# Performance work log

Measured on AMD Instinct MI355X. Metric: run time of the kernel, lower is better.

The kernel has to match this reference:

```python
import jax, jax.numpy as jnp
import numpy as np

F32 = jnp.float32

def denorm_px(pts, H, W):
    # kornia denormalize_pixel_coordinates: [-1,1] -> pixel
    x = (pts[..., 0] + 1.0) * (W - 1) * 0.5
    y = (pts[..., 1] + 1.0) * (H - 1) * 0.5
    return jnp.stack([x, y], axis=-1)

def norm_px(pts, H, W):
    x = pts[..., 0] * 2.0 / (W - 1) - 1.0
    y = pts[..., 1] * 2.0 / (H - 1) - 1.0
    return jnp.stack([x, y], axis=-1)

def conv2d_same(x, k, mode):
    # depthwise 2d conv, 'same' output, border via jnp.pad mode
    kh, kw = k.shape
    ph, pw = kh // 2, kw // 2
    xp = jnp.pad(x, ((0, 0), (0, 0), (ph, ph), (pw, pw)), mode=mode)
    C = x.shape[1]
    kern = jnp.broadcast_to(k[None, None], (C, 1, kh, kw)).astype(x.dtype)
    return jax.lax.conv_general_dilated(xp, kern, (1, 1), 'VALID',
        dimension_numbers=('NCHW', 'OIHW', 'NCHW'), feature_group_count=C)

def nms2d(x, k=5):
    p = k // 2
    m = jax.lax.reduce_window(x, -jnp.inf, jax.lax.max, (1, 1, k, k), (1, 1, 1, 1),
                              [(0, 0), (0, 0), (p, p), (p, p)])
    return jnp.where(x == m, x, 0.0)

def gaussian_kernel2d(ksize=7, sigma=1.0):
    ax = jnp.arange(ksize, dtype=F32) - (ksize - 1) / 2.0
    g = jnp.exp(-0.5 * (ax / sigma) ** 2)
    g = g / g.sum()
    return jnp.outer(g, g)

def gftt_response(gray):
    # kornia CornerGFTT: normalized sobel grads, blurred structure tensor, min-eig
    sx = jnp.array([[-1, 0, 1], [-2, 0, 2], [-1, 0, 1]], F32) / 8.0
    gx = conv2d_same(gray, sx, 'edge')
    gy = conv2d_same(gray, sx.T, 'edge')
    g = gaussian_kernel2d(7, 1.0)
    dx2 = conv2d_same(gx * gx, g, 'reflect')
    dy2 = conv2d_same(gy * gy, g, 'reflect')
    dxy = conv2d_same(gx * gy, g, 'reflect')
    tr = dx2 + dy2
    disc = jnp.sqrt(jnp.clip((dx2 - dy2) ** 2 + 4.0 * dxy ** 2, 0.0))
    return 0.5 * (tr - disc)

def laplacian5(x):
    k = jnp.ones((5, 5), F32).at[2, 2].set(1.0 - 25.0)
    k = k / jnp.abs(k).sum()  # kornia normalized laplacian kernel
    return conv2d_same(x, k, 'reflect')

def pairwise_project(pts, depths, poses, K):
    # pts [B,N,2] normalized; poses [B,4,4] cam-to-world
    # returns proj [B(dst),B(src),N,2] normalized + vis [B,B,N]
    B, N, _ = pts.shape
    H, W = depths.shape[-2:]
    px = denorm_px(pts, H, W)
    xi = jnp.clip(jnp.round(px[..., 0]), 0, W - 1).astype(jnp.int32)
    yi = jnp.clip(jnp.round(px[..., 1]), 0, H - 1).astype(jnp.int32)
    d = depths[jnp.arange(B)[:, None], 0, yi, xi]  # [B,N]
    Kinv = jnp.linalg.inv(K)
    hom = jnp.concatenate([px, jnp.ones_like(px[..., :1])], axis=-1)
    cam = (hom @ Kinv.T) * d[..., None]  # [B,N,3]
    R, t = poses[:, :3, :3], poses[:, :3, 3]
    world = jnp.einsum('bij,bnj->bni', R, cam) + t[:, None]
    diff = world[None] - t[:, None, None]  # [i,j,n,3]
    cam2 = jnp.einsum('iab,ijna->ijnb', R, diff)  # R_i^T (world - t_i)
    uvw = cam2 @ K.T
    z = uvw[..., 2]
    zs = jnp.where(jnp.abs(z) > 1e-6, z, 1e-6)
    u, v = uvw[..., 0] / zs, uvw[..., 1] / zs
    vis = (z > 0.1) & (u >= 0) & (u <= W - 1) & (v >= 0) & (v <= H - 1)
    return norm_px(jnp.stack([u, v], -1), H, W), vis

def pairwise_cosine_inter(x, y, eps=1e-8):
    xx = jnp.sum(x * x, -1)
    yy = jnp.sum(y * y, -1)
    xy = jnp.einsum('amd,bnd->abmn', x, y)
    den = jnp.sqrt(jnp.clip(xx[:, None, :, None] * yy[None, :, None, :], eps * eps))
    return xy / den

def pairwise_cosine_intra(x, y, eps=1e-8):
    xx = jnp.sum(x * x, -1)
    yy = jnp.sum(y * y, -1)
    xy = jnp.einsum('bmd,bnd->bmn', x, y)
    den = jnp.sqrt(jnp.clip(xx[..., :, None] * yy[..., None, :], eps * eps))
    return xy / den

def distinction_loss(desc):
    return jnp.maximum(pairwise_cosine_intra(desc, desc), 0.0).mean()

def match_loss(desc, points, proj, vis, H, W, radius=1.0):
    B, N, _ = points.shape
    src = denorm_px(jax.lax.stop_gradient(points), H, W)  # [b,m,2]
    dst = denorm_px(jax.lax.stop_gradient(proj), H, W)  # [a,b,n,2]
    x2 = jnp.sum(src * src, -1)  # [b,m]
    y2 = jnp.sum(dst * dst, -1)  # [a,b,n]
    xy = jnp.einsum('bmd,abnd->abmn', src, dst)
    dist = jnp.sqrt(jnp.clip(x2[None, :, :, None] + y2[:, :, None, :] - 2.0 * xy, 0.0))
    valid = vis[:, :, :, None]  # torch: dist[invis rows] = nan -> excluded from both masks
    tri = jnp.triu(jnp.ones((N, N), bool), 1)
    pcos = pairwise_cosine_inter(desc, desc)
    mpos = (dist <= radius) & tri & valid
    mneg = (dist > radius) & tri & valid
    pos_mean = jnp.sum(jnp.where(mpos, pcos, 0.0)) / jnp.maximum(mpos.sum(), 1)
    neg_mean = jnp.sum(jnp.where(mneg, pcos, 0.0)) / jnp.maximum(mneg.sum(), 1)
    return 1.0 - pos_mean + neg_mean

def get_corner_target(imgs, depths, poses, K, num_corners=500, radius=8):
    B, _, H, W = imgs.shape
    gray = 0.299 * imgs[:, 0:1] + 0.587 * imgs[:, 1:2] + 0.114 * imgs[:, 2:3]
    corners = nms2d(gftt_response(gray), 5)
    # MaxPool(8, return_indices) + MaxUnpool(8): keep only per-8x8-block max
    xr = corners.reshape(B, 1, H // radius, radius, W // radius, radius)
    bm = xr.max(axis=(3, 5), keepdims=True)
    keep = jnp.where(xr == bm, xr, 0.0).reshape(B, 1, H, W)
    values, idx = jax.lax.top_k(keep.reshape(B, -1), num_corners)  # [B,Nc]
    coords = jnp.stack([idx % W, idx // W], axis=2).astype(F32)  # (x,y)
    coords = norm_px(coords, H, W)
    proj, vis = pairwise_project(coords, depths, poses, K)  # [B,B,Nc,2]
    proj = jnp.where(vis[..., None], proj, -2.0)
    comb = jnp.transpose(proj, (1, 0, 2, 3)).reshape(B, B * num_corners, 2)
    px = jnp.round(denorm_px(comb, H, W)).astype(jnp.int32)
    wf = px[..., 0].reshape(-1)
    hf = px[..., 1].reshape(-1)
    bf = jnp.repeat(jnp.arange(B), B * num_corners)
    vals = jnp.tile(values.reshape(-1), B)
    mask = (wf >= 0) & (hf >= 0) & (wf < W) & (hf < H)
    vals = jnp.where(mask, vals, 0.0)
    wf = jnp.clip(wf, 0, W - 1)
    hf = jnp.clip(hf, 0, H - 1)
    target = jnp.zeros_like(corners).at[bf, 0, hf, wf].max(vals)
    target = nms2d(target, 5)
    return jax.lax.stop_gradient((target > 0).astype(F32))

def score_loss(scores, imgs, depths, poses, K):
    target = get_corner_target(imgs, depths, poses, K)
    p = jnp.clip(scores, 1e-12, 1.0 - 1e-12)
    bce = -(target * jnp.log(p) + (1.0 - target) * jnp.log(1.0 - p)).mean()
    lap = laplacian5(scores)
    return bce + (scores * jnp.exp(-lap)).mean() * 10.0

def featurenet_loss(descriptors, points, pointness, depths_dense, poses, K, imgs):
    beta = (1.0, 0.5, 1.0)
    H, W = pointness.shape[2], pointness.shape[3]
    distinction = distinction_loss(descriptors)
    cornerness = score_loss(pointness, imgs, depths_dense, poses, K)
    proj_pts, vis = pairwise_project(points, depths_dense, poses, K)
    match = match_loss(descriptors, points, proj_pts, vis, H, W, radius=1.0)
    return beta[0] * distinction + beta[1] * cornerness + beta[2] * match

def setup_inputs() -> dict:
    key = jax.random.key(0)
    ks = jax.random.split(key, 6)
    B, N, D, H, W = 6, 1024, 128, 320, 320
    descriptors = jax.random.normal(ks[0], (B, N, D), F32)
    points = jax.random.uniform(ks[1], (B, N, 2), F32, -0.9, 0.9)
    pointness = jax.random.uniform(ks[2], (B, 1, H, W), F32, 1e-3, 1.0 - 1e-3)
    depths_dense = jax.random.uniform(ks[3], (B, 1, H, W), F32, 1.0, 6.0)
    t = jax.random.uniform(ks[4], (B, 3), F32, -0.2, 0.2)
    poses = jnp.tile(jnp.eye(4, dtype=F32), (B, 1, 1)).at[:, :3, 3].set(t)
    K = jnp.array([[float(W), 0.0, W / 2.0], [0.0, float(W), H / 2.0], [0.0, 0.0, 1.0]], F32)
    imgs = jax.random.uniform(ks[5], (B, 3, H, W), F32)
    return dict(descriptors=descriptors, points=points, pointness=pointness,
                depths_dense=depths_dense, poses=poses, K=K, imgs=imgs)

def reference(descriptors, points, pointness, depths_dense, poses, K, imgs):
    return featurenet_loss(descriptors, points, pointness, depths_dense, poses, K, imgs)
```

## Files before the change

### kernel.cpp

```cpp
#include <hip/hip_runtime.h>
#include <stdint.h>

#define BB 6
#define NPTS 1024
#define DD 128
#define HH 320
#define WW 320
#define NC 500
#define HWsz (HH*WW)
#define CAP 2048
#define NBLK ((HH/8)*(WW/8))
#define TX 32
#define TY 8
#define NSLOT 64

typedef __attribute__((ext_vector_type(8))) short bf16x8;
typedef __attribute__((ext_vector_type(4))) float f32x4;

__device__ __forceinline__ int clampi(int v, int lo, int hi){ return v<lo?lo:(v>hi?hi:v); }
__device__ __forceinline__ int refl(int p, int L){ if(p<0)p=-p; if(p>=L)p=2*L-2-p; return p; }

__device__ __forceinline__ float wave_sum(float v){
  #pragma unroll
  for (int o = 32; o > 0; o >>= 1) v += __shfl_xor(v, o, 64);
  return v;
}
__device__ __forceinline__ double wave_sumd(double v){
  #pragma unroll
  for (int o = 32; o > 0; o >>= 1) v += __shfl_xor(v, o, 64);
  return v;
}
__device__ __forceinline__ float wave_max(float v){
  #pragma unroll
  for (int o = 32; o > 0; o >>= 1) v = fmaxf(v, __shfl_xor(v, o, 64));
  return v;
}

__device__ __constant__ float GW[7] = {
  0.0044330481f, 0.0540055850f, 0.2420362300f, 0.3990502700f,
  0.2420362300f, 0.0540055850f, 0.0044330481f };

struct Proj { float u, v; int vis; };

__device__ Proj project_point(float ptx, float pty, int jsrc, int itgt,
                              const float* __restrict__ depths,
                              const float* __restrict__ poses,
                              const float* __restrict__ Km)
{
  float pxx = ((ptx + 1.0f)*(float)(WW-1))*0.5f;
  float pxy = ((pty + 1.0f)*(float)(HH-1))*0.5f;
  float rx = rintf(pxx), ry = rintf(pxy);
  rx = fminf(fmaxf(rx, 0.f), (float)(WW-1));
  ry = fminf(fmaxf(ry, 0.f), (float)(HH-1));
  int xi = (int)rx, yi = (int)ry;
  float d = depths[(size_t)jsrc*HWsz + yi*WW + xi];
  float a00=Km[0],a01=Km[1],a02=Km[2],a10=Km[3],a11=Km[4],a12=Km[5],a20=Km[6],a21=Km[7],a22=Km[8];
  float det = a00*(a11*a22 - a12*a21) - a01*(a10*a22 - a12*a20) + a02*(a10*a21 - a11*a20);
  float id_ = 1.0f/det;
  float i00 = (a11*a22 - a12*a21)*id_;
  float i01 = (a02*a21 - a01*a22)*id_;
  float i02 = (a01*a12 - a02*a11)*id_;
  float i10 = (a12*a20 - a10*a22)*id_;
  float i11 = (a00*a22 - a02*a20)*id_;
  float i12 = (a02*a10 - a00*a12)*id_;
  float i20 = (a10*a21 - a11*a20)*id_;
  float i21 = (a01*a20 - a00*a21)*id_;
  float i22 = (a00*a11 - a01*a10)*id_;
  float c0 = (i00*pxx + i01*pxy + i02)*d;
  float c1 = (i10*pxx + i11*pxy + i12)*d;
  float c2 = (i20*pxx + i21*pxy + i22)*d;
  const float* Pj = poses + (size_t)jsrc*16;
  float w0 = Pj[0]*c0 + Pj[1]*c1 + Pj[2]*c2  + Pj[3];
  float w1 = Pj[4]*c0 + Pj[5]*c1 + Pj[6]*c2  + Pj[7];
  float w2 = Pj[8]*c0 + Pj[9]*c1 + Pj[10]*c2 + Pj[11];
  const float* Pi = poses + (size_t)itgt*16;
  float dx = w0 - Pi[3], dy = w1 - Pi[7], dz = w2 - Pi[11];
  float e0 = Pi[0]*dx + Pi[4]*dy + Pi[8]*dz;
  float e1 = Pi[1]*dx + Pi[5]*dy + Pi[9]*dz;
  float e2 = Pi[2]*dx + Pi[6]*dy + Pi[10]*dz;
  float uu = a00*e0 + a01*e1 + a02*e2;
  float vv = a10*e0 + a11*e1 + a12*e2;
  float zz = a20*e0 + a21*e1 + a22*e2;
  float zs = (fabsf(zz) > 1e-6f) ? zz : 1e-6f;
  Proj r;
  r.u = uu/zs; r.v = vv/zs;
  r.vis = (zz > 0.1f) && (r.u >= 0.f) && (r.u <= (float)(WW-1)) && (r.v >= 0.f) && (r.v <= (float)(HH-1));
  return r;
}

__global__ __launch_bounds__(256) void k_graysobel(const float* __restrict__ imgs,
        float* __restrict__ gxx, float* __restrict__ gyy, float* __restrict__ gxy){
  __shared__ float lg[TY+2][TX+2];
  int b = blockIdx.z;
  int x0 = blockIdx.x*TX, y0 = blockIdx.y*TY;
  const float* br = imgs + (size_t)b*3*HWsz;
  const float* bg = br + HWsz;
  const float* bb = bg + HWsz;
  const int W2 = TX+2, H2 = TY+2;
  for (int i = threadIdx.x; i < H2*W2; i += 256){
    int ly = i / W2, lx = i - ly*W2;
    int gy = clampi(y0 - 1 + ly, 0, HH-1), gx = clampi(x0 - 1 + lx, 0, WW-1);
    size_t off = (size_t)gy*WW + gx;
    lg[ly][lx] = 0.299f*br[off] + 0.587f*bg[off] + 0.114f*bb[off];
  }
  __syncthreads();
  int tx = threadIdx.x & (TX-1), ty = threadIdx.x / TX;
  float g00 = lg[ty][tx],   g01 = lg[ty][tx+1],   g02 = lg[ty][tx+2];
  float g10 = lg[ty+1][tx],                        g12 = lg[ty+1][tx+2];
  float g20 = lg[ty+2][tx], g21 = lg[ty+2][tx+1], g22 = lg[ty+2][tx+2];
  float gx = 0.125f*(g02-g00) + 0.25f*(g12-g10) + 0.125f*(g22-g20);
  float gy = 0.125f*(g20-g00) + 0.25f*(g21-g01) + 0.125f*(g22-g02);
  size_t o = (size_t)b*HWsz + (size_t)(y0+ty)*WW + (x0+tx);
  gxx[o] = gx*gx; gyy[o] = gy*gy; gxy[o] = gx*gy;
}

__global__ __launch_bounds__(256) void k_gauss_resp(const float* __restrict__ gxx,
        const float* __restrict__ gyy, const float* __restrict__ gxy, float* __restrict__ resp){
  __shared__ float lxx[TY+6][TX+6], lyy[TY+6][TX+6], lxy[TY+6][TX+6];
  int b = blockIdx.z;
  int x0 = blockIdx.x*TX, y0 = blockIdx.y*TY;
  const float* axx = gxx + (size_t)b*HWsz;
  const float* ayy = gyy + (size_t)b*HWsz;
  const float* axy = gxy + (size_t)b*HWsz;
  const int W2 = TX+6, H2 = TY+6;
  for (int i = threadIdx.x; i < H2*W2; i += 256){
    int ly = i / W2, lx = i - ly*W2;
    int gy = refl(y0 - 3 + ly, HH), gx = refl(x0 - 3 + lx, WW);
    size_t off = (size_t)gy*WW + gx;
    lxx[ly][lx] = axx[off]; lyy[ly][lx] = ayy[off]; lxy[ly][lx] = axy[off];
  }
  __syncthreads();
  int tx = threadIdx.x & (TX-1), ty = threadIdx.x / TX;
  float sxx=0.f, syy=0.f, sxy=0.f;
  #pragma unroll
  for (int i=0;i<7;++i){
    float wr = GW[i];
    #pragma unroll
    for (int j=0;j<7;++j){
      float wc = wr*GW[j];
      sxx += wc*lxx[ty+i][tx+j];
      syy += wc*lyy[ty+i][tx+j];
      sxy += wc*lxy[ty+i][tx+j];
    }
  }
  float tr = sxx+syy, df = sxx-syy;
  float disc = sqrtf(fmaxf(df*df + 4.f*sxy*sxy, 0.f));
  resp[(size_t)b*HWsz + (size_t)(y0+ty)*WW + (x0+tx)] = 0.5f*(tr - disc);
}

__global__ __launch_bounds__(256) void k_nmsblk(const float* __restrict__ resp,
        unsigned long long* __restrict__ ckeys, unsigned int* __restrict__ ccnt){
  __shared__ float lr[TY+4][TX+4];
  __shared__ float lk[TY][TX];
  int b = blockIdx.z;
  int x0 = blockIdx.x*TX, y0 = blockIdx.y*TY;
  const float* rb = resp + (size_t)b*HWsz;
  const int W2 = TX+4, H2 = TY+4;
  for (int i = threadIdx.x; i < H2*W2; i += 256){
    int ly = i / W2, lx = i - ly*W2;
    int gy = y0 - 2 + ly, gx = x0 - 2 + lx;
    lr[ly][lx] = (gy >= 0 && gy < HH && gx >= 0 && gx < WW) ? rb[(size_t)gy*WW + gx] : -1e30f;
  }
  __syncthreads();
  int tx = threadIdx.x & (TX-1), ty = threadIdx.x / TX;
  float m = -1e30f;
  #pragma unroll
  for (int dy=0; dy<5; ++dy)
    #pragma unroll
    for (int dx=0; dx<5; ++dx) m = fmaxf(m, lr[ty+dy][tx+dx]);
  float r = lr[ty+2][tx+2];
  lk[ty][tx] = (r == m) ? r : 0.f;
  __syncthreads();
  int wave = threadIdx.x >> 6, lane = threadIdx.x & 63;
  int ly = lane >> 3, lx = wave*8 + (lane & 7);
  float v = lk[ly][lx];
  float bm = wave_max(v);
  if (!(bm > 0.f)) return;
  unsigned long long mask = __ballot(v == bm);
  if (v == bm){
    int yy = y0 + ly, xx2 = x0 + lx;
    unsigned long long key =
      ((unsigned long long)__float_as_uint(bm) << 32) |
      (unsigned long long)(0xFFFFFFFFu - (unsigned int)(yy*WW + xx2));
    int rank = __popcll(mask & ((1ull << lane) - 1ull));
    int rblk = blockIdx.y*(WW/8) + blockIdx.x*4 + wave;
    if (rank == 0){
      ckeys[(size_t)b*CAP + rblk] = key;
    } else {
      unsigned int slot = NBLK + atomicAdd(&ccnt[b], 1u);
      if (slot < CAP) ckeys[(size_t)b*CAP + slot] = key;
    }
  }
}

__global__ __launch_bounds__(1024) void k_top500(const unsigned long long* __restrict__ ckeys,
        float* __restrict__ cpts, float* __restrict__ cvals){
  __shared__ unsigned long long sk[CAP];
  int b = blockIdx.x;
  int tid = threadIdx.x;
  for (int i = tid; i < CAP; i += 1024)
    sk[i] = ckeys[(size_t)b*CAP + i];
  __syncthreads();
  for (int k = 2; k <= CAP; k <<= 1){
    for (int j = k >> 1; j > 0; j >>= 1){
      for (int i = tid; i < CAP; i += 1024){
        int l = i ^ j;
        if (l > i){
          unsigned long long A = sk[i], Bv = sk[l];
          bool up = ((i & k) == 0);
          if ((A > Bv) == up){ sk[i] = Bv; sk[l] = A; }
        }
      }
      __syncthreads();
    }
  }
  if (tid < NC){
    unsigned long long key = sk[CAP-1-tid];
    float val = __uint_as_float((unsigned int)(key >> 32));
    size_t o = (size_t)b*NC + tid;
    if (val > 0.f){
      unsigned int idx = 0xFFFFFFFFu - (unsigned int)(key & 0xFFFFFFFFull);
      float fx = (float)(idx % WW), fy = (float)(idx / WW);
      cpts[o*2+0] = (fx*2.0f)/(float)(WW-1) - 1.0f;
      cpts[o*2+1] = (fy*2.0f)/(float)(HH-1) - 1.0f;
      cvals[o] = val;
    } else {
      cpts[o*2+0] = __int_as_float(0x7fc00000);
      cpts[o*2+1] = __int_as_float(0x7fc00000);
      cvals[o] = 0.f;
    }
  }
}

__global__ void k_corner_scatter(const float* __restrict__ cpts, const float* __restrict__ cvals,
        const float* __restrict__ depths, const float* __restrict__ poses,
        const float* __restrict__ Km, unsigned int* __restrict__ target){
  int t = blockIdx.x*blockDim.x + threadIdx.x;
  if (t >= BB*BB*NC) return;
  int i = t / (BB*NC); int r = t - i*(BB*NC); int j = r / NC; int n = r - j*NC;
  float val = cvals[(size_t)i*NC + n];
  float ptx = cpts[((size_t)j*NC+n)*2+0];
  float pty = cpts[((size_t)j*NC+n)*2+1];
  if (!(val > 0.f) || ptx != ptx) return;
  Proj pr = project_point(ptx, pty, j, i, depths, poses, Km);
  if (!pr.vis) return;
  float nu = (pr.u*2.0f)/(float)(WW-1) - 1.0f;
  float nv = (pr.v*2.0f)/(float)(HH-1) - 1.0f;
  float px2 = ((nu+1.0f)*(float)(WW-1))*0.5f;
  float py2 = ((nv+1.0f)*(float)(HH-1))*0.5f;
  float rx = rintf(px2), ry = rintf(py2);
  if (!(rx >= 0.f && ry >= 0.f && rx <= (float)(WW-1) && ry <= (float)(HH-1))) return;
  int wf = (int)rx, hf = (int)ry;
  atomicMax(&target[(size_t)j*HWsz + hf*WW + wf], __float_as_uint(val));
}

__global__ __launch_bounds__(256) void k_score_reduce(const float* __restrict__ target,
        const float* __restrict__ scores, double* __restrict__ accs){
  __shared__ float ltg[TY+4][TX+4], lsc[TY+4][TX+4];
  __shared__ float rbuf[4][2];
  int b = blockIdx.z;
  int x0 = blockIdx.x*TX, y0 = blockIdx.y*TY;
  const float* tg = target + (size_t)b*HWsz;
  const float* sb = scores + (size_t)b*HWsz;
  const int W2 = TX+4, H2 = TY+4;
  for (int i = threadIdx.x; i < H2*W2; i += 256){
    int ly = i / W2, lx = i - ly*W2;
    int gy = y0 - 2 + ly, gx = x0 - 2 + lx;
    ltg[ly][lx] = (gy >= 0 && gy < HH && gx >= 0 && gx < WW) ? tg[(size_t)gy*WW + gx] : -1e30f;
    lsc[ly][lx] = sb[(size_t)refl(gy,HH)*WW + refl(gx,WW)];
  }
  __syncthreads();
  int tx = threadIdx.x & (TX-1), ty = threadIdx.x / TX;
  float m = -1e30f, S5 = 0.f;
  #pragma unroll
  for (int dy=0; dy<5; ++dy)
    #pragma unroll
    for (int dx=0; dx<5; ++dx){
      m = fmaxf(m, ltg[ty+dy][tx+dx]);
      S5 += lsc[ty+dy][tx+dx];
    }
  float tv = ltg[ty+2][tx+2];
  float sc = lsc[ty+2][tx+2];
  float tb = (tv > 0.f && tv == m) ? 1.f : 0.f;
  float pc = fminf(fmaxf(sc, 1e-12f), 1.0f - 1e-12f);
  float bce = -(tb*logf(pc) + (1.f-tb)*logf(1.f-pc));
  float lap = (S5 - sc)*(1.0f/48.0f) - 0.5f*sc;
  float extra = sc*expf(-lap);
  bce = wave_sum(bce); extra = wave_sum(extra);
  int wave = threadIdx.x >> 6, lane = threadIdx.x & 63;
  if (lane == 0){ rbuf[wave][0] = bce; rbuf[wave][1] = extra; }
  __syncthreads();
  if (threadIdx.x == 0){
    int slot = (blockIdx.x + blockIdx.y*(WW/TX) + blockIdx.z*400) & (NSLOT-1);
    atomicAdd(&accs[(1*NSLOT + slot)*8], (double)(rbuf[0][0]+rbuf[1][0]+rbuf[2][0]+rbuf[3][0]));
    atomicAdd(&accs[(2*NSLOT + slot)*8], (double)(rbuf[0][1]+rbuf[1][1]+rbuf[2][1]+rbuf[3][1]));
  }
}

__global__ void k_rowproj(const float* __restrict__ desc, float* __restrict__ xx,
        unsigned short* __restrict__ dbf,
        const float* __restrict__ points, const float* __restrict__ depths,
        const float* __restrict__ poses, const float* __restrict__ Km,
        float* __restrict__ mproj, unsigned char* __restrict__ mvis){
  int t = blockIdx.x*blockDim.x + threadIdx.x;
  if (t < BB*NPTS){
    const float* dptr = desc + (size_t)t*DD;
    unsigned short* optr = dbf + (size_t)t*DD;
    float s = 0.f;
    for (int d = 0; d < DD; d += 4){
      float4 v = *(const float4*)(dptr + d);
      s += v.x*v.x + v.y*v.y + v.z*v.z + v.w*v.w;
      unsigned int u0 = __float_as_uint(v.x); optr[d+0] = (unsigned short)((u0 + 0x7fffu + ((u0>>16)&1u)) >> 16);
      unsigned int u1 = __float_as_uint(v.y); optr[d+1] = (unsigned short)((u1 + 0x7fffu + ((u1>>16)&1u)) >> 16);
      unsigned int u2 = __float_as_uint(v.z); optr[d+2] = (unsigned short)((u2 + 0x7fffu + ((u2>>16)&1u)) >> 16);
      unsigned int u3 = __float_as_uint(v.w); optr[d+3] = (unsigned short)((u3 + 0x7fffu + ((u3>>16)&1u)) >> 16);
    }
    xx[t] = s;
    return;
  }
  int t2 = t - BB*NPTS;
  if (t2 >= BB*BB*NPTS) return;
  int i = t2 / (BB*NPTS); int r = t2 - i*(BB*NPTS); int j = r / NPTS; int n = r - j*NPTS;
  float ptx = points[((size_t)j*NPTS+n)*2+0];
  float pty = points[((size_t)j*NPTS+n)*2+1];
  Proj pr = project_point(ptx, pty, j, i, depths, poses, Km);
  mproj[(size_t)t2*2+0] = (pr.u*2.0f)/(float)(WW-1) - 1.0f;
  mproj[(size_t)t2*2+1] = (pr.v*2.0f)/(float)(HH-1) - 1.0f;
  mvis[t2] = pr.vis ? 1 : 0;
}

__global__ __launch_bounds__(256) void k_distinction_mfma(const unsigned short* __restrict__ dbf,
        const float* __restrict__ xx, double* __restrict__ accs){
  __shared__ float rbuf[4];
  int b = blockIdx.z;
  int tid = threadIdx.x;
  int wave = tid >> 6, lane = tid & 63;
  int wr = blockIdx.x*64 + (wave&1)*32;
  int wc = blockIdx.y*64 + (wave>>1)*32;
  int r = lane & 15, kg = lane >> 4;
  const unsigned short* descb = dbf + (size_t)b*NPTS*DD;
  const float* xb = xx + (size_t)b*NPTS;
  f32x4 c00 = {}, c01 = {}, c10 = {}, c11 = {};
  #pragma unroll
  for (int ks = 0; ks < 4; ++ks){
    int ko = ks*32 + kg*8;
    bf16x8 a0 = *(const bf16x8*)(descb + (size_t)(wr+r)*DD + ko);
    bf16x8 a1 = *(const bf16x8*)(descb + (size_t)(wr+16+r)*DD + ko);
    bf16x8 b0 = *(const bf16x8*)(descb + (size_t)(wc+r)*DD + ko);
    bf16x8 b1 = *(const bf16x8*)(descb + (size_t)(wc+16+r)*DD + ko);
    c00 = __builtin_amdgcn_mfma_f32_16x16x32_bf16(a0, b0, c00, 0, 0, 0);
    c01 = __builtin_amdgcn_mfma_f32_16x16x32_bf16(a0, b1, c01, 0, 0, 0);
    c10 = __builtin_amdgcn_mfma_f32_16x16x32_bf16(a1, b0, c10, 0, 0, 0);
    c11 = __builtin_amdgcn_mfma_f32_16x16x32_bf16(a1, b1, c11, 0, 0, 0);
  }
  float xn0 = xb[wc + r], xn1 = xb[wc + 16 + r];
  float local = 0.f;
  #pragma unroll
  for (int mi = 0; mi < 2; ++mi){
    #pragma unroll
    for (int j = 0; j < 4; ++j){
      float xm = xb[wr + mi*16 + 4*kg + j];
      float v0 = (mi ? c10[j] : c00[j]);
      float v1 = (mi ? c11[j] : c01[j]);
      local += fmaxf(v0 * rsqrtf(fmaxf(xm*xn0, 1e-16f)), 0.f);
      local += fmaxf(v1 * rsqrtf(fmaxf(xm*xn1, 1e-16f)), 0.f);
    }
  }
  local = wave_sum(local);
  if (lane == 0) rbuf[wave] = local;
  __syncthreads();
  if (tid == 0){
    int slot = (blockIdx.x + blockIdx.y*16 + blockIdx.z*32) & (NSLOT-1);
    atomicAdd(&accs[(0*NSLOT + slot)*8], (double)(rbuf[0]+rbuf[1]+rbuf[2]+rbuf[3]));
  }
}

__global__ __launch_bounds__(256) void k_match_mfma(const unsigned short* __restrict__ dbf,
        const float* __restrict__ xx, const float* __restrict__ points,
        const float* __restrict__ mproj, const unsigned char* __restrict__ mvis,
        double* __restrict__ accs){
  __shared__ float rbuf[4][4];
  int ab = blockIdx.z; int a = ab / BB, b = ab - a*BB;
  int ti = blockIdx.x;
  int mt = 0;
  while (ti >= 16 - mt){ ti -= 16 - mt; ++mt; }
  int nt = mt + ti;
  int tid = threadIdx.x;
  int wave = tid >> 6, lane = tid & 63;
  int wr = mt*64 + (wave&1)*32;
  int wc = nt*64 + (wave>>1)*32;
  int r = lane & 15, kg = lane >> 4;
  const unsigned short* descA = dbf + (size_t)a*NPTS*DD;
  const unsigned short* descB = dbf + (size_t)b*NPTS*DD;
  const float* xxa = xx + (size_t)a*NPTS;
  const float* xxb = xx + (size_t)b*NPTS;
  const float* pts = points + (size_t)b*NPTS*2;
  const float* mp  = mproj + (((size_t)a*BB+b)*NPTS)*2;
  const unsigned char* mv = mvis + ((size_t)a*BB+b)*NPTS;
  f32x4 c00 = {}, c01 = {}, c10 = {}, c11 = {};
  #pragma unroll
  for (int ks = 0; ks < 4; ++ks){
    int ko = ks*32 + kg*8;
    bf16x8 a0 = *(const bf16x8*)(descA + (size_t)(wr+r)*DD + ko);
    bf16x8 a1 = *(const bf16x8*)(descA + (size_t)(wr+16+r)*DD + ko);
    bf16x8 b0 = *(const bf16x8*)(descB + (size_t)(wc+r)*DD + ko);
    bf16x8 b1 = *(const bf16x8*)(descB + (size_t)(wc+16+r)*DD + ko);
    c00 = __builtin_amdgcn_mfma_f32_16x16x32_bf16(a0, b0, c00, 0, 0, 0);
    c01 = __builtin_amdgcn_mfma_f32_16x16x32_bf16(a0, b1, c01, 0, 0, 0);
    c10 = __builtin_amdgcn_mfma_f32_16x16x32_bf16(a1, b0, c10, 0, 0, 0);
    c11 = __builtin_amdgcn_mfma_f32_16x16x32_bf16(a1, b1, c11, 0, 0, 0);
  }
  float nxxv[2], ndx[2], ndy[2], ny2[2];
  #pragma unroll
  for (int ni = 0; ni < 2; ++ni){
    int n = wc + ni*16 + r;
    nxxv[ni] = xxb[n];
    float qx = mp[n*2+0], qy = mp[n*2+1];
    float dx = ((qx+1.f)*(float)(WW-1))*0.5f;
    float dy = ((qy+1.f)*(float)(HH-1))*0.5f;
    ndx[ni] = dx; ndy[ni] = dy;
    ny2[ni] = dx*dx + dy*dy;
  }
  float pos = 0.f, neg = 0.f, pcf = 0.f, ncf = 0.f;
  #pragma unroll
  for (int mi = 0; mi < 2; ++mi){
    #pragma unroll
    for (int j = 0; j < 4; ++j){
      int m = wr + mi*16 + 4*kg + j;
      if (!mv[m]) continue;
      float px = pts[m*2+0], py = pts[m*2+1];
      float sx = ((px+1.f)*(float)(WW-1))*0.5f;
      float sy = ((py+1.f)*(float)(HH-1))*0.5f;
      float x2 = sx*sx + sy*sy;
      float xm = xxa[m];
      #pragma unroll
      for (int ni = 0; ni < 2; ++ni){
        int n = wc + ni*16 + r;
        if (m >= n) continue;
        float dv = (mi ? (ni ? c11[j] : c10[j]) : (ni ? c01[j] : c00[j]));
        float d2 = x2 + ny2[ni] - 2.f*(sx*ndx[ni] + sy*ndy[ni]);
        float p = dv * rsqrtf(fmaxf(xm * nxxv[ni], 1e-16f));
        if (d2 <= 1.0f){ pos += p; pcf += 1.f; }
        else           { neg += p; ncf += 1.f; }
      }
    }
  }
  pos = wave_sum(pos); neg = wave_sum(neg);
  pcf = wave_sum(pcf); ncf = wave_sum(ncf);
  if (lane == 0){ rbuf[wave][0] = pos; rbuf[wave][1] = neg; rbuf[wave][2] = pcf; rbuf[wave][3] = ncf; }
  __syncthreads();
  if (tid == 0){
    int slot = (blockIdx.x + blockIdx.z*8) & (NSLOT-1);
    atomicAdd(&accs[(3*NSLOT + slot)*8], (double)(rbuf[0][0]+rbuf[1][0]+rbuf[2][0]+rbuf[3][0]));
    atomicAdd(&accs[(4*NSLOT + slot)*8], (double)(rbuf[0][1]+rbuf[1][1]+rbuf[2][1]+rbuf[3][1]));
    atomicAdd(&accs[(5*NSLOT + slot)*8], (double)(rbuf[0][2]+rbuf[1][2]+rbuf[2][2]+rbuf[3][2]));
    atomicAdd(&accs[(6*NSLOT + slot)*8], (double)(rbuf[0][3]+rbuf[1][3]+rbuf[2][3]+rbuf[3][3]));
  }
}

__global__ void k_final(const double* __restrict__ accs, float* __restrict__ out){
  int lane = threadIdx.x;
  double tot[7];
  #pragma unroll
  for (int q = 0; q < 7; ++q)
    tot[q] = wave_sumd(accs[((size_t)q*NSLOT + lane)*8]);
  if (lane == 0){
    double distinction = tot[0] / (double)((long long)BB*NPTS*NPTS);
    double bce = tot[1] / (double)((long long)BB*HWsz);
    double extra = tot[2] / (double)((long long)BB*HWsz);
    double cornerness = bce + 10.0*extra;
    double pcd = tot[5] < 0.5 ? 1.0 : tot[5];
    double ncd = tot[6] < 0.5 ? 1.0 : tot[6];
    double pos_mean = tot[3] / pcd;
    double neg_mean = tot[4] / ncd;
    double match = 1.0 - pos_mean + neg_mean;
    out[0] = (float)(distinction + 0.5*cornerness + match);
  }
}

extern "C" void kernel_launch(void* const* d_in, const int* in_sizes, int n_in,
                              void* d_out, int out_size, void* d_ws, size_t ws_size,
                              hipStream_t stream) {
  (void)in_sizes; (void)n_in; (void)out_size; (void)ws_size;
  const float* desc   = (const float*)d_in[0];
  const float* points = (const float*)d_in[1];
  const float* scores = (const float*)d_in[2];
  const float* depths = (const float*)d_in[3];
  const float* poses  = (const float*)d_in[4];
  const float* Km     = (const float*)d_in[5];
  const float* imgs   = (const float*)d_in[6];
  float* out = (float*)d_out;

  const size_t S = (size_t)BB*HWsz;
  float* resp = (float*)d_ws;
  float* gxx  = resp + S;
  float* gyy  = gxx + S;
  float* gxy  = gyy + S;
  unsigned long long* ckeys = (unsigned long long*)(gxy + S);
  unsigned int* ccnt = (unsigned int*)(ckeys + (size_t)BB*CAP);
  double* accs = (double*)(ccnt + 8);
  float* cpts  = (float*)(accs + 7*NSLOT*8);
  float* cvals = cpts + (size_t)BB*NC*2;
  float* xx    = cvals + (size_t)BB*NC;
  float* mproj = xx + (size_t)BB*NPTS;
  unsigned char* mvis = (unsigned char*)(mproj + (size_t)BB*BB*NPTS*2);
  unsigned short* dbf = (unsigned short*)(mvis + (size_t)BB*BB*NPTS);

  dim3 blk(256);
  dim3 gtile(WW/TX, HH/TY, BB);

  k_graysobel<<<gtile, blk, 0, stream>>>(imgs, gxx, gyy, gxy);
  k_gauss_resp<<<gtile, blk, 0, stream>>>(gxx, gyy, gxy, resp);

  hipMemsetAsync(gyy, 0, S*sizeof(float), stream);
  hipMemsetAsync(ckeys, 0,
      (size_t)BB*CAP*sizeof(unsigned long long) + 8*sizeof(unsigned int) +
      (size_t)7*NSLOT*8*sizeof(double), stream);

  k_nmsblk<<<gtile, blk, 0, stream>>>(resp, ckeys, ccnt);
  k_top500<<<dim3(BB), dim3(1024), 0, stream>>>(ckeys, cpts, cvals);
  {
    int n = BB*BB*NC;
    k_corner_scatter<<<dim3((n+255)/256), blk, 0, stream>>>(cpts, cvals, depths, poses, Km,
                                                            (unsigned int*)gyy);
  }
  k_score_reduce<<<gtile, blk, 0, stream>>>(gyy, scores, accs);
  {
    int n = BB*NPTS + BB*BB*NPTS;
    k_rowproj<<<dim3((n+255)/256), blk, 0, stream>>>(desc, xx, dbf, points, depths, poses, Km,
                                                     mproj, mvis);
  }
  k_distinction_mfma<<<dim3(16, 16, BB), blk, 0, stream>>>(dbf, xx, accs);
  k_match_mfma<<<dim3(136, 1, BB*BB), blk, 0, stream>>>(dbf, xx, points, mproj, mvis, accs);
  k_final<<<dim3(1), dim3(64), 0, stream>>>(accs, out);
}
```

Measured before the change: 215.3 us.

## Fuse gray/Sobel into Gaussian response kernel and merge distinction into match GEMM

Gray conversion, Sobel and the structure-tensor blur now run in one kernel, so the three gradient-product planes no longer go through global memory and two memsets become one. The distinction Gram computation moves into the match kernel: its first 1536 blocks do both tiles, which removes a launch. The per-point loads in the match kernel are also hoisted ahead of the MFMA loop to overlap their latency. In exchange the fused kernel recomputes halo gradients and uses more shared memory, and the merged kernel's block work is uneven.

```diff
diff --git a/kernel.cpp b/kernel.cpp
--- a/kernel.cpp
+++ b/kernel.cpp
@@ -88,46 +88,35 @@
   return r;
 }
 
-__global__ __launch_bounds__(256) void k_graysobel(const float* __restrict__ imgs,
-        float* __restrict__ gxx, float* __restrict__ gyy, float* __restrict__ gxy){
-  __shared__ float lg[TY+2][TX+2];
+__global__ __launch_bounds__(256) void k_gftt(const float* __restrict__ imgs,
+        float* __restrict__ resp){
+  __shared__ float lg[TY+8][TX+8];
+  __shared__ float lxx[TY+6][TX+6], lyy[TY+6][TX+6], lxy[TY+6][TX+6];
   int b = blockIdx.z;
   int x0 = blockIdx.x*TX, y0 = blockIdx.y*TY;
   const float* br = imgs + (size_t)b*3*HWsz;
   const float* bg = br + HWsz;
-  const float* bb = bg + HWsz;
-  const int W2 = TX+2, H2 = TY+2;
-  for (int i = threadIdx.x; i < H2*W2; i += 256){
-    int ly = i / W2, lx = i - ly*W2;
-    int gy = clampi(y0 - 1 + ly, 0, HH-1), gx = clampi(x0 - 1 + lx, 0, WW-1);
+  const float* bbl = bg + HWsz;
+  const int GW2 = TX+8, GH2 = TY+8;
+  for (int i = threadIdx.x; i < GH2*GW2; i += 256){
+    int ly = i / GW2, lx = i - ly*GW2;
+    int gy = clampi(y0-4+ly, 0, HH-1), gx = clampi(x0-4+lx, 0, WW-1);
     size_t off = (size_t)gy*WW + gx;
-    lg[ly][lx] = 0.299f*br[off] + 0.587f*bg[off] + 0.114f*bb[off];
-  }
-  __syncthreads();
-  int tx = threadIdx.x & (TX-1), ty = threadIdx.x / TX;
-  float g00 = lg[ty][tx],   g01 = lg[ty][tx+1],   g02 = lg[ty][tx+2];
-  float g10 = lg[ty+1][tx],                        g12 = lg[ty+1][tx+2];
-  float g20 = lg[ty+2][tx], g21 = lg[ty+2][tx+1], g22 = lg[ty+2][tx+2];
-  float gx = 0.125f*(g02-g00) + 0.25f*(g12-g10) + 0.125f*(g22-g20);
-  float gy = 0.125f*(g20-g00) + 0.25f*(g21-g01) + 0.125f*(g22-g02);
-  size_t o = (size_t)b*HWsz + (size_t)(y0+ty)*WW + (x0+tx);
-  gxx[o] = gx*gx; gyy[o] = gy*gy; gxy[o] = gx*gy;
-}
-
-__global__ __launch_bounds__(256) void k_gauss_resp(const float* __restrict__ gxx,
-        const float* __restrict__ gyy, const float* __restrict__ gxy, float* __restrict__ resp){
-  __shared__ float lxx[TY+6][TX+6], lyy[TY+6][TX+6], lxy[TY+6][TX+6];
-  int b = blockIdx.z;
-  int x0 = blockIdx.x*TX, y0 = blockIdx.y*TY;
-  const float* axx = gxx + (size_t)b*HWsz;
-  const float* ayy = gyy + (size_t)b*HWsz;
-  const float* axy = gxy + (size_t)b*HWsz;
-  const int W2 = TX+6, H2 = TY+6;
-  for (int i = threadIdx.x; i < H2*W2; i += 256){
-    int ly = i / W2, lx = i - ly*W2;
-    int gy = refl(y0 - 3 + ly, HH), gx = refl(x0 - 3 + lx, WW);
-    size_t off = (size_t)gy*WW + gx;
-    lxx[ly][lx] = axx[off]; lyy[ly][lx] = ayy[off]; lxy[ly][lx] = axy[off];
+    lg[ly][lx] = 0.299f*br[off] + 0.587f*bg[off] + 0.114f*bbl[off];
+  }
+  __syncthreads();
+  const int PW2 = TX+6, PH2 = TY+6;
+  for (int i = threadIdx.x; i < PH2*PW2; i += 256){
+    int ly = i / PW2, lx = i - ly*PW2;
+    int pcy = refl(y0-3+ly, HH), pcx = refl(x0-3+lx, WW);
+    int ym = clampi(pcy-1,0,HH-1)-(y0-4), yc = pcy-(y0-4), yp = clampi(pcy+1,0,HH-1)-(y0-4);
+    int xm = clampi(pcx-1,0,WW-1)-(x0-4), xc = pcx-(x0-4), xp = clampi(pcx+1,0,WW-1)-(x0-4);
+    float g00=lg[ym][xm], g01=lg[ym][xc], g02=lg[ym][xp];
+    float g10=lg[yc][xm],                 g12=lg[yc][xp];
+    float g20=lg[yp][xm], g21=lg[yp][xc], g22=lg[yp][xp];
+    float gx = 0.125f*(g02-g00)+0.25f*(g12-g10)+0.125f*(g22-g20);
+    float gy = 0.125f*(g20-g00)+0.25f*(g21-g01)+0.125f*(g22-g02);
+    lxx[ly][lx]=gx*gx; lyy[ly][lx]=gy*gy; lxy[ly][lx]=gx*gy;
   }
   __syncthreads();
   int tx = threadIdx.x & (TX-1), ty = threadIdx.x / TX;
@@ -329,53 +318,7 @@
   mvis[t2] = pr.vis ? 1 : 0;
 }
 
-__global__ __launch_bounds__(256) void k_distinction_mfma(const unsigned short* __restrict__ dbf,
-        const float* __restrict__ xx, double* __restrict__ accs){
-  __shared__ float rbuf[4];
-  int b = blockIdx.z;
-  int tid = threadIdx.x;
-  int wave = tid >> 6, lane = tid & 63;
-  int wr = blockIdx.x*64 + (wave&1)*32;
-  int wc = blockIdx.y*64 + (wave>>1)*32;
-  int r = lane & 15, kg = lane >> 4;
-  const unsigned short* descb = dbf + (size_t)b*NPTS*DD;
-  const float* xb = xx + (size_t)b*NPTS;
-  f32x4 c00 = {}, c01 = {}, c10 = {}, c11 = {};
-  #pragma unroll
-  for (int ks = 0; ks < 4; ++ks){
-    int ko = ks*32 + kg*8;
-    bf16x8 a0 = *(const bf16x8*)(descb + (size_t)(wr+r)*DD + ko);
-    bf16x8 a1 = *(const bf16x8*)(descb + (size_t)(wr+16+r)*DD + ko);
-    bf16x8 b0 = *(const bf16x8*)(descb + (size_t)(wc+r)*DD + ko);
-    bf16x8 b1 = *(const bf16x8*)(descb + (size_t)(wc+16+r)*DD + ko);
-    c00 = __builtin_amdgcn_mfma_f32_16x16x32_bf16(a0, b0, c00, 0, 0, 0);
-    c01 = __builtin_amdgcn_mfma_f32_16x16x32_bf16(a0, b1, c01, 0, 0, 0);
-    c10 = __builtin_amdgcn_mfma_f32_16x16x32_bf16(a1, b0, c10, 0, 0, 0);
-    c11 = __builtin_amdgcn_mfma_f32_16x16x32_bf16(a1, b1, c11, 0, 0, 0);
-  }
-  float xn0 = xb[wc + r], xn1 = xb[wc + 16 + r];
-  float local = 0.f;
-  #pragma unroll
-  for (int mi = 0; mi < 2; ++mi){
-    #pragma unroll
-    for (int j = 0; j < 4; ++j){
-      float xm = xb[wr + mi*16 + 4*kg + j];
-      float v0 = (mi ? c10[j] : c00[j]);
-      float v1 = (mi ? c11[j] : c01[j]);
-      local += fmaxf(v0 * rsqrtf(fmaxf(xm*xn0, 1e-16f)), 0.f);
-      local += fmaxf(v1 * rsqrtf(fmaxf(xm*xn1, 1e-16f)), 0.f);
-    }
-  }
-  local = wave_sum(local);
-  if (lane == 0) rbuf[wave] = local;
-  __syncthreads();
-  if (tid == 0){
-    int slot = (blockIdx.x + blockIdx.y*16 + blockIdx.z*32) & (NSLOT-1);
-    atomicAdd(&accs[(0*NSLOT + slot)*8], (double)(rbuf[0]+rbuf[1]+rbuf[2]+rbuf[3]));
-  }
-}
-
-__global__ __launch_bounds__(256) void k_match_mfma(const unsigned short* __restrict__ dbf,
+__global__ __launch_bounds__(256) void k_grams(const unsigned short* __restrict__ dbf,
         const float* __restrict__ xx, const float* __restrict__ points,
         const float* __restrict__ mproj, const unsigned char* __restrict__ mvis,
         double* __restrict__ accs){
@@ -397,6 +340,33 @@
   const float* pts = points + (size_t)b*NPTS*2;
   const float* mp  = mproj + (((size_t)a*BB+b)*NPTS)*2;
   const unsigned char* mv = mvis + ((size_t)a*BB+b)*NPTS;
+  float nxxv[2], ndx[2], ndy[2], ny2[2];
+  #pragma unroll
+  for (int ni = 0; ni < 2; ++ni){
+    int n = wc + ni*16 + r;
+    nxxv[ni] = xxb[n];
+    float qx = mp[n*2+0], qy = mp[n*2+1];
+    float dx = ((qx+1.f)*(float)(WW-1))*0.5f;
+    float dy = ((qy+1.f)*(float)(HH-1))*0.5f;
+    ndx[ni] = dx; ndy[ni] = dy;
+    ny2[ni] = dx*dx + dy*dy;
+  }
+  bool  mok[2][4];
+  float msx[2][4], msy[2][4], mx2[2][4], mxv[2][4];
+  #pragma unroll
+  for (int mi = 0; mi < 2; ++mi){
+    #pragma unroll
+    for (int j = 0; j < 4; ++j){
+      int m = wr + mi*16 + 4*kg + j;
+      mok[mi][j] = (mv[m] != 0);
+      float px = pts[m*2+0], py = pts[m*2+1];
+      float sx = ((px+1.f)*(float)(WW-1))*0.5f;
+      float sy = ((py+1.f)*(float)(HH-1))*0.5f;
+      msx[mi][j] = sx; msy[mi][j] = sy;
+      mx2[mi][j] = sx*sx + sy*sy;
+      mxv[mi][j] = xxa[m];
+    }
+  }
   f32x4 c00 = {}, c01 = {}, c10 = {}, c11 = {};
   #pragma unroll
   for (int ks = 0; ks < 4; ++ks){
@@ -410,29 +380,15 @@
     c10 = __builtin_amdgcn_mfma_f32_16x16x32_bf16(a1, b0, c10, 0, 0, 0);
     c11 = __builtin_amdgcn_mfma_f32_16x16x32_bf16(a1, b1, c11, 0, 0, 0);
   }
-  float nxxv[2], ndx[2], ndy[2], ny2[2];
-  #pragma unroll
-  for (int ni = 0; ni < 2; ++ni){
-    int n = wc + ni*16 + r;
-    nxxv[ni] = xxb[n];
-    float qx = mp[n*2+0], qy = mp[n*2+1];
-    float dx = ((qx+1.f)*(float)(WW-1))*0.5f;
-    float dy = ((qy+1.f)*(float)(HH-1))*0.5f;
-    ndx[ni] = dx; ndy[ni] = dy;
-    ny2[ni] = dx*dx + dy*dy;
-  }
   float pos = 0.f, neg = 0.f, pcf = 0.f, ncf = 0.f;
   #pragma unroll
   for (int mi = 0; mi < 2; ++mi){
     #pragma unroll
     for (int j = 0; j < 4; ++j){
       int m = wr + mi*16 + 4*kg + j;
-      if (!mv[m]) continue;
-      float px = pts[m*2+0], py = pts[m*2+1];
-      float sx = ((px+1.f)*(float)(WW-1))*0.5f;
-      float sy = ((py+1.f)*(float)(HH-1))*0.5f;
-      float x2 = sx*sx + sy*sy;
-      float xm = xxa[m];
+      if (!mok[mi][j]) continue;
+      float sx = msx[mi][j], sy = msy[mi][j];
+      float x2 = mx2[mi][j], xm = mxv[mi][j];
       #pragma unroll
       for (int ni = 0; ni < 2; ++ni){
         int n = wc + ni*16 + r;
@@ -455,6 +411,48 @@
     atomicAdd(&accs[(4*NSLOT + slot)*8], (double)(rbuf[0][1]+rbuf[1][1]+rbuf[2][1]+rbuf[3][1]));
     atomicAdd(&accs[(5*NSLOT + slot)*8], (double)(rbuf[0][2]+rbuf[1][2]+rbuf[2][2]+rbuf[3][2]));
     atomicAdd(&accs[(6*NSLOT + slot)*8], (double)(rbuf[0][3]+rbuf[1][3]+rbuf[2][3]+rbuf[3][3]));
+  }
+  int flat = blockIdx.x + 136*blockIdx.z;
+  if (flat >= 1536) return;
+  int db = flat >> 8;
+  int dt = flat & 255;
+  int wr2 = (dt >> 4)*64 + (wave&1)*32;
+  int wc2 = (dt & 15)*64 + (wave>>1)*32;
+  const unsigned short* descb = dbf + (size_t)db*NPTS*DD;
+  const float* xb = xx + (size_t)db*NPTS;
+  f32x4 e00 = {}, e01 = {}, e10 = {}, e11 = {};
+  #pragma unroll
+  for (int ks = 0; ks < 4; ++ks){
+    int ko = ks*32 + kg*8;
+    bf16x8 a0 = *(const bf16x8*)(descb + (size_t)(wr2+r)*DD + ko);
+    bf16x8 a1 = *(const bf16x8*)(descb + (size_t)(wr2+16+r)*DD + ko);
+    bf16x8 b0 = *(const bf16x8*)(descb + (size_t)(wc2+r)*DD + ko);
+    bf16x8 b1 = *(const bf16x8*)(descb + (size_t)(wc2+16+r)*DD + ko);
+    e00 = __builtin_amdgcn_mfma_f32_16x16x32_bf16(a0, b0, e00, 0, 0, 0);
+    e01 = __builtin_amdgcn_mfma_f32_16x16x32_bf16(a0, b1, e01, 0, 0, 0);
+    e10 = __builtin_amdgcn_mfma_f32_16x16x32_bf16(a1, b0, e10, 0, 0, 0);
+    e11 = __builtin_amdgcn_mfma_f32_16x16x32_bf16(a1, b1, e11, 0, 0, 0);
+  }
+  float xn0 = xb[wc2 + r], xn1 = xb[wc2 + 16 + r];
+  float local = 0.f;
+  #pragma unroll
+  for (int mi = 0; mi < 2; ++mi){
+    #pragma unroll
+    for (int j = 0; j < 4; ++j){
+      float xm = xb[wr2 + mi*16 + 4*kg + j];
+      float v0 = (mi ? e10[j] : e00[j]);
+      float v1 = (mi ? e11[j] : e01[j]);
+      local += fmaxf(v0 * rsqrtf(fmaxf(xm*xn0, 1e-16f)), 0.f);
+      local += fmaxf(v1 * rsqrtf(fmaxf(xm*xn1, 1e-16f)), 0.f);
+    }
+  }
+  local = wave_sum(local);
+  __syncthreads();
+  if (lane == 0) rbuf[wave][0] = local;
+  __syncthreads();
+  if (tid == 0){
+    int slot = flat & (NSLOT-1);
+    atomicAdd(&accs[(0*NSLOT + slot)*8], (double)(rbuf[0][0]+rbuf[1][0]+rbuf[2][0]+rbuf[3][0]));
   }
 }
 
@@ -492,11 +490,9 @@
   float* out = (float*)d_out;
 
   const size_t S = (size_t)BB*HWsz;
-  float* resp = (float*)d_ws;
-  float* gxx  = resp + S;
-  float* gyy  = gxx + S;
-  float* gxy  = gyy + S;
-  unsigned long long* ckeys = (unsigned long long*)(gxy + S);
+  float* resp   = (float*)d_ws;
+  float* target = resp + S;
+  unsigned long long* ckeys = (unsigned long long*)(target + S);
   unsigned int* ccnt = (unsigned int*)(ckeys + (size_t)BB*CAP);
   double* accs = (double*)(ccnt + 8);
   float* cpts  = (float*)(accs + 7*NSLOT*8);
@@ -509,28 +505,25 @@
   dim3 blk(256);
   dim3 gtile(WW/TX, HH/TY, BB);
 
-  k_graysobel<<<gtile, blk, 0, stream>>>(imgs, gxx, gyy, gxy);
-  k_gauss_resp<<<gtile, blk, 0, stream>>>(gxx, gyy, gxy, resp);
-
-  hipMemsetAsync(gyy, 0, S*sizeof(float), stream);
-  hipMemsetAsync(ckeys, 0,
+  hipMemsetAsync(target, 0,
+      S*sizeof(float) +
       (size_t)BB*CAP*sizeof(unsigned long long) + 8*sizeof(unsigned int) +
       (size_t)7*NSLOT*8*sizeof(double), stream);
 
+  k_gftt<<<gtile, blk, 0, stream>>>(imgs, resp);
   k_nmsblk<<<gtile, blk, 0, stream>>>(resp, ckeys, ccnt);
   k_top500<<<dim3(BB), dim3(1024), 0, stream>>>(ckeys, cpts, cvals);
   {
     int n = BB*BB*NC;
     k_corner_scatter<<<dim3((n+255)/256), blk, 0, stream>>>(cpts, cvals, depths, poses, Km,
-                                                            (unsigned int*)gyy);
-  }
-  k_score_reduce<<<gtile, blk, 0, stream>>>(gyy, scores, accs);
+                                                            (unsigned int*)target);
+  }
+  k_score_reduce<<<gtile, blk, 0, stream>>>(target, scores, accs);
   {
     int n = BB*NPTS + BB*BB*NPTS;
     k_rowproj<<<dim3((n+255)/256), blk, 0, stream>>>(desc, xx, dbf, points, depths, poses, Km,
                                                      mproj, mvis);
   }
-  k_distinction_mfma<<<dim3(16, 16, BB), blk, 0, stream>>>(dbf, xx, accs);
-  k_match_mfma<<<dim3(136, 1, BB*BB), blk, 0, stream>>>(dbf, xx, points, mproj, mvis, accs);
+  k_grams<<<dim3(136, 1, BB*BB), blk, 0, stream>>>(dbf, xx, points, mproj, mvis, accs);
   k_final<<<dim3(1), dim3(64), 0, stream>>>(accs, out);
 }
```

New measurement: 198.1 us. 8.0% less time.
